# Performance work log

Hardware: AMD Instinct MI355X
Metric: run time of the kernel (lower is better)

## Reference

```python
import jax, jax.numpy as jnp
import numpy as np

N_HEAD = 16
N_EMBD = 1024
D_HEAD = N_EMBD // N_HEAD


def setup_inputs() -> dict:
    key = jax.random.key(0)
    ks = jax.random.split(key, 5)
    B, T, C = 4, 2048, N_EMBD
    s = 1.0 / np.sqrt(C)
    return {
        "x": jax.random.normal(ks[0], (B, T, C), dtype=jnp.float32),
        "w_qkv": jax.random.normal(ks[1], (C, 3 * C), dtype=jnp.float32) * s,
        "b_qkv": jnp.zeros((3 * C,), dtype=jnp.float32),
        "w_out": jax.random.normal(ks[2], (C, C), dtype=jnp.float32) * s,
        "b_out": jnp.zeros((C,), dtype=jnp.float32),
    }


def reference(x, w_qkv, b_qkv, w_out, b_out):
    B, T, C = x.shape
    qkv = x @ w_qkv + b_qkv  # [B,T,3C]
    q, k, v = jnp.split(qkv, 3, axis=-1)
    # [B,T,C] -> [B,H,T,D]
    def heads(t):
        return t.reshape(B, T, N_HEAD, D_HEAD).transpose(0, 2, 1, 3)
    q, k, v = heads(q), heads(k), heads(v)
    scores = jnp.einsum("bhqd,bhkd->bhqk", q, k) / np.sqrt(D_HEAD)
    causal = jnp.tril(jnp.ones((T, T), dtype=bool))
    scores = jnp.where(causal, scores, -jnp.inf)
    probs = jax.nn.softmax(scores, axis=-1)
    out = jnp.einsum("bhqk,bhkd->bhqd", probs, v)  # [B,H,T,D]
    out = out.transpose(0, 2, 1, 3).reshape(B, T, C)
    return out @ w_out + b_out
```

## Files before the change

kernel.cpp:

```cpp
#include <hip/hip_runtime.h>
#include <hip/hip_bf16.h>
#include <cstdint>
#include <cstddef>

typedef __attribute__((ext_vector_type(8))) short short8;
typedef __attribute__((ext_vector_type(4))) float f32x4;
typedef __attribute__((ext_vector_type(4))) uint16_t ushort4_t;
typedef __attribute__((ext_vector_type(4))) uint32_t uint4_t;

__device__ __forceinline__ uint16_t f2bf(float f) {
  union { float f; uint32_t u; } v; v.f = f;
  uint32_t r = v.u + 0x7FFFu + ((v.u >> 16) & 1u);
  return (uint16_t)(r >> 16);
}


__global__ __launch_bounds__(256) void cvt_f32_bf16(const float* __restrict__ in,
                                                    uint16_t* __restrict__ out, int n4) {
  int i = blockIdx.x * 256 + threadIdx.x;
  int stride = gridDim.x * 256;
  for (; i < n4; i += stride) {
    float4 v = ((const float4*)in)[i];
    ushort4_t o = { f2bf(v.x), f2bf(v.y), f2bf(v.z), f2bf(v.w) };
    ((ushort4_t*)out)[i] = o;
  }
}

__global__ __launch_bounds__(256) void transpose_cvt(const float* __restrict__ in,
                                                     uint16_t* __restrict__ out, int R, int C) {
  __shared__ float tile[32][33];
  int c0 = blockIdx.x * 32, r0 = blockIdx.y * 32;
  int tx = threadIdx.x, ty = threadIdx.y;
#pragma unroll
  for (int j = 0; j < 32; j += 8)
    tile[ty + j][tx] = in[(size_t)(r0 + ty + j) * C + c0 + tx];
  __syncthreads();
#pragma unroll
  for (int j = 0; j < 32; j += 8)
    out[(size_t)(c0 + ty + j) * R + r0 + tx] = f2bf(tile[tx][ty + j]);
}

__global__ __launch_bounds__(256) void transpose_v(const uint16_t* __restrict__ in,
                                                   uint16_t* __restrict__ out) {
  __shared__ uint16_t tile[32][33];
  int bh = blockIdx.z;
  int t0 = blockIdx.x * 32, d0 = blockIdx.y * 32;
  const uint16_t* ip = in + (size_t)bh * 2048 * 64;
  uint16_t* op = out + (size_t)bh * 64 * 2048;
  int tx = threadIdx.x, ty = threadIdx.y;
#pragma unroll
  for (int j = 0; j < 32; j += 8)
    tile[ty + j][tx] = ip[(size_t)(t0 + ty + j) * 64 + d0 + tx];
  __syncthreads();
  const int txp = (tx < 16) ? ((tx >> 2) * 8 + (tx & 3))
                            : (((tx - 16) >> 2) * 8 + 4 + (tx & 3));
#pragma unroll
  for (int j = 0; j < 32; j += 8)
    op[(size_t)(d0 + ty + j) * 2048 + t0 + txp] = tile[tx][ty + j];
}

__device__ __forceinline__ void stage16(const uint16_t* g, uint16_t* lds) {
  __builtin_amdgcn_global_load_lds((__attribute__((address_space(1))) void*)g,
                                   (__attribute__((address_space(3))) void*)lds, 16, 0, 0);
}

__global__ __launch_bounds__(256, 3) void gemm_qkv(
    const uint16_t* __restrict__ A, const uint16_t* __restrict__ Bt,
    const float* __restrict__ bias,
    uint16_t* __restrict__ q_out, uint16_t* __restrict__ k_out, uint16_t* __restrict__ v_out) {
  constexpr int K = 1024, KT = 16;
  __shared__ uint16_t lA[256 * 64];
  __shared__ uint16_t lB[128 * 64];
  const int tid = threadIdx.x;
  const int lane = tid & 63, w = tid >> 6;
  const int wm = w >> 1, wn = w & 1;
  const int r16 = lane & 15, hi = lane >> 4;
  const int wg = (blockIdx.x & 7) * 96 + (blockIdx.x >> 3);
  const int bm = wg / 24, bn = wg % 24;

  const int row0 = tid >> 3;
  const int cch0 = (tid & 7) ^ (row0 & 7);
  const uint16_t* aS = A + ((size_t)bm * 256 + row0) * K + cch0 * 8;
  const uint16_t* bS = Bt + ((size_t)bn * 128 + row0) * K + cch0 * 8;

  f32x4 acc[8][4];
#pragma unroll
  for (int m = 0; m < 8; ++m)
#pragma unroll
    for (int n = 0; n < 4; ++n) acc[m][n] = (f32x4){0.f, 0.f, 0.f, 0.f};

#pragma unroll 1
  for (int kt = 0; kt < KT; ++kt) {
#pragma unroll
    for (int it = 0; it < 8; ++it)
      stage16(aS + (size_t)(it * 32) * K + kt * 64, &lA[it * 2048 + tid * 8]);
#pragma unroll
    for (int it = 0; it < 4; ++it)
      stage16(bS + (size_t)(it * 32) * K + kt * 64, &lB[it * 2048 + tid * 8]);
    __syncthreads();

#pragma unroll
    for (int kk = 0; kk < 2; ++kk) {
      short8 bfr[4];
      const int swz = (kk * 64 + hi * 16) ^ ((r16 & 7) << 4);
#pragma unroll
      for (int n = 0; n < 4; ++n) {
        int rowb = wn * 64 + n * 16 + r16;
        bfr[n] = *(const short8*)((const char*)lB + rowb * 128 + swz);
      }
#pragma unroll
      for (int mh = 0; mh < 2; ++mh) {
        short8 af[4];
#pragma unroll
        for (int i = 0; i < 4; ++i) {
          int rowa = wm * 128 + mh * 64 + i * 16 + r16;
          af[i] = *(const short8*)((const char*)lA + rowa * 128 + swz);
        }
        __builtin_amdgcn_s_setprio(1);
#pragma unroll
        for (int i = 0; i < 4; ++i)
#pragma unroll
          for (int n = 0; n < 4; ++n)
            acc[mh * 4 + i][n] =
                __builtin_amdgcn_mfma_f32_16x16x32_bf16(af[i], bfr[n], acc[mh * 4 + i][n], 0, 0, 0);
        __builtin_amdgcn_s_setprio(0);
      }
    }
    __syncthreads();
  }

#pragma unroll
  for (int m = 0; m < 8; ++m) {
    int rg = bm * 256 + wm * 128 + (m >> 2) * 64 + (m & 3) * 16 + hi * 4;
#pragma unroll
    for (int n = 0; n < 4; ++n) {
      int cg = bn * 128 + wn * 64 + n * 16 + r16;
      float bv = bias[cg];
      int which = cg >> 10, hh = (cg >> 6) & 15, dd = cg & 63;
      uint16_t* dst = which == 0 ? q_out : (which == 1 ? k_out : v_out);
#pragma unroll
      for (int r = 0; r < 4; ++r) {
        int rgr = rg + r;
        dst[((size_t)((rgr >> 11) * 16 + hh) * 2048 + (rgr & 2047)) * 64 + dd] = f2bf(acc[m][n][r] + bv);
      }
    }
  }
}


__global__ __launch_bounds__(256) void gemm128_out(
    const uint16_t* __restrict__ A, const uint16_t* __restrict__ Bt,
    const float* __restrict__ bias, int K, float* __restrict__ f_out, int N) {
  __shared__ uint16_t lA[128 * 64];
  __shared__ uint16_t lB[128 * 64];
  const int tid = threadIdx.x;
  const int lane = tid & 63;
  const int w = tid >> 6, wm = w >> 1, wn = w & 1;
  const int r16 = lane & 15, hi = lane >> 4;
  const int bn = blockIdx.x, bm = blockIdx.y;

  f32x4 acc[4][4];
#pragma unroll
  for (int i = 0; i < 4; ++i)
#pragma unroll
    for (int j = 0; j < 4; ++j) acc[i][j] = (f32x4){0.f, 0.f, 0.f, 0.f};

  const int ksteps = K >> 6;
  for (int kt = 0; kt < ksteps; ++kt) {
#pragma unroll
    for (int it = 0; it < 4; ++it) {
      int ci = it * 256 + tid;
      int row = ci >> 3;
      int cch = (ci & 7) ^ (row & 7);
      stage16(A + (size_t)(bm * 128 + row) * K + kt * 64 + cch * 8, &lA[ci * 8]);
      stage16(Bt + (size_t)(bn * 128 + row) * K + kt * 64 + cch * 8, &lB[ci * 8]);
    }
    __syncthreads();
#pragma unroll
    for (int kk = 0; kk < 2; ++kk) {
      short8 af[4], bfr[4];
      int swz = (kk * 64 + hi * 16) ^ ((r16 & 7) << 4);
#pragma unroll
      for (int i = 0; i < 4; ++i) {
        int rowa = wm * 64 + i * 16 + r16;
        af[i] = *(const short8*)((const char*)lA + rowa * 128 + swz);
        int rowb = wn * 64 + i * 16 + r16;
        bfr[i] = *(const short8*)((const char*)lB + rowb * 128 + swz);
      }
#pragma unroll
      for (int i = 0; i < 4; ++i)
#pragma unroll
        for (int j = 0; j < 4; ++j)
          acc[i][j] = __builtin_amdgcn_mfma_f32_16x16x32_bf16(af[i], bfr[j], acc[i][j], 0, 0, 0);
    }
    __syncthreads();
  }

#pragma unroll
  for (int i = 0; i < 4; ++i) {
    int rbase = bm * 128 + wm * 64 + i * 16 + hi * 4;
#pragma unroll
    for (int j = 0; j < 4; ++j) {
      int cg = bn * 128 + wn * 64 + j * 16 + r16;
      float bv = bias[cg];
#pragma unroll
      for (int r = 0; r < 4; ++r)
        f_out[(size_t)(rbase + r) * N + cg] = acc[i][j][r] + bv;
    }
  }
}

__global__ __launch_bounds__(256, 3) void attn_fwd(
    const uint16_t* __restrict__ Qm, const uint16_t* __restrict__ Km,
    const uint16_t* __restrict__ Vt, uint16_t* __restrict__ O) {
  __shared__ uint16_t kbuf[2][64 * 64];
  __shared__ uint16_t vbuf[2][64 * 64];
  const int tid = threadIdx.x;
  const int lane = tid & 63, w = tid >> 6;
  const int r16 = lane & 15, hi = lane >> 4;
  const int bid = blockIdx.x;
  const int bh = (bid & 7) + 8 * ((bid >> 3) & 7);
  const int qb = 15 - (bid >> 6);
  const int b = bh >> 4, h = bh & 15;
  const size_t base = (size_t)bh * 2048 * 64;
  const int qlo = qb * 128 + w * 32;
  const int NT = 2 * qb + 2;

  const float SC = 0.18033688011112042f;
  const float BIAS = -20.197730572445487f;

  short8 ones8;
#pragma unroll
  for (int i = 0; i < 8; ++i) ones8[i] = (short)0x3F80;

  short8 aq[2][2];
#pragma unroll
  for (int st = 0; st < 2; ++st)
#pragma unroll
    for (int c = 0; c < 2; ++c)
      aq[st][c] = *(const short8*)&Qm[base + (size_t)(qlo + st * 16 + r16) * 64 + c * 32 + hi * 8];

  f32x4 o[2][4];
  f32x4 o4[2];
#pragma unroll
  for (int st = 0; st < 2; ++st) {
#pragma unroll
    for (int j = 0; j < 4; ++j) o[st][j] = (f32x4){0.f, 0.f, 0.f, 0.f};
    o4[st] = (f32x4){0.f, 0.f, 0.f, 0.f};
  }

  auto stage_tile = [&](int pb, int kv0) {
    {
      int c = tid;            int row = c >> 3, cch = (c & 7) ^ (row & 7);
      stage16(Km + base + (size_t)(kv0 + row) * 64 + cch * 8, &kbuf[pb][c * 8]);
    }
    {
      int c = tid + 256;      int row = c >> 3, cch = (c & 7) ^ (row & 7);
      stage16(Km + base + (size_t)(kv0 + row) * 64 + cch * 8, &kbuf[pb][c * 8]);
    }
    {
      int c = tid;            int row = c >> 3, cch = (c & 7) ^ (row & 7);
      stage16(Vt + base + (size_t)row * 2048 + kv0 + cch * 8, &vbuf[pb][c * 8]);
    }
    {
      int c = tid + 256;      int row = c >> 3, cch = (c & 7) ^ (row & 7);
      stage16(Vt + base + (size_t)row * 2048 + kv0 + cch * 8, &vbuf[pb][c * 8]);
    }
  };

  int pb = 0;
  stage_tile(0, 0);
#pragma unroll 1
  for (int t = 0; t < NT; ++t) {
    const int kv0 = t << 6;
    if (t + 1 < NT) {
      stage_tile(pb ^ 1, (t + 1) << 6);
      asm volatile("s_waitcnt vmcnt(4)" ::: "memory");
    } else {
      asm volatile("s_waitcnt vmcnt(0)" ::: "memory");
    }
    __builtin_amdgcn_s_barrier();
    __builtin_amdgcn_sched_barrier(0);

    if (kv0 <= qlo + 31) {
      const bool maskt = (kv0 + 64 > qlo);
      short8 bk[4][2];
#pragma unroll
      for (int ct = 0; ct < 4; ++ct)
#pragma unroll
        for (int c = 0; c < 2; ++c) {
          int row = ct * 16 + r16;
          int ch = (c * 4 + hi) ^ (row & 7);
          bk[ct][c] = *(const short8*)((const char*)&kbuf[pb][0] + row * 128 + ch * 16);
        }
      short8 bv[4][2];
#pragma unroll
      for (int j = 0; j < 4; ++j)
#pragma unroll
        for (int ks = 0; ks < 2; ++ks) {
          int row = j * 16 + r16;
          int ch = (ks * 4 + hi) ^ (row & 7);
          bv[j][ks] = *(const short8*)((const char*)&vbuf[pb][0] + row * 128 + ch * 16);
        }

#pragma unroll
      for (int st = 0; st < 2; ++st) {
        f32x4 sc[4];
#pragma unroll
        for (int ct = 0; ct < 4; ++ct) sc[ct] = (f32x4){0.f, 0.f, 0.f, 0.f};
        __builtin_amdgcn_s_setprio(1);
#pragma unroll
        for (int ct = 0; ct < 4; ++ct)
#pragma unroll
          for (int c = 0; c < 2; ++c)
            sc[ct] = __builtin_amdgcn_mfma_f32_16x16x32_bf16(bk[ct][c], aq[st][c], sc[ct], 0, 0, 0);
        __builtin_amdgcn_s_setprio(0);

        float p[4][4];
        const int qg = qlo + st * 16 + r16;
#pragma unroll
        for (int ct = 0; ct < 4; ++ct) {
          const int kb_ = kv0 + ct * 16 + hi * 4;
#pragma unroll
          for (int r = 0; r < 4; ++r) {
            float x = exp2f(fmaf(sc[ct][r], SC, BIAS));
            if (maskt && (kb_ + r > qg)) x = 0.f;
            p[ct][r] = x;
          }
        }

        short8 pf[2];
#pragma unroll
        for (int ks = 0; ks < 2; ++ks) {
          uint32_t d0, d1, d2, d3;
          asm("v_cvt_pk_bf16_f32 %0, %1, %2" : "=v"(d0) : "v"(p[2 * ks][0]), "v"(p[2 * ks][1]));
          asm("v_cvt_pk_bf16_f32 %0, %1, %2" : "=v"(d1) : "v"(p[2 * ks][2]), "v"(p[2 * ks][3]));
          asm("v_cvt_pk_bf16_f32 %0, %1, %2" : "=v"(d2) : "v"(p[2 * ks + 1][0]), "v"(p[2 * ks + 1][1]));
          asm("v_cvt_pk_bf16_f32 %0, %1, %2" : "=v"(d3) : "v"(p[2 * ks + 1][2]), "v"(p[2 * ks + 1][3]));
          uint4_t uu = { d0, d1, d2, d3 };
          pf[ks] = __builtin_bit_cast(short8, uu);
        }

        __builtin_amdgcn_s_setprio(1);
#pragma unroll
        for (int ks = 0; ks < 2; ++ks)
          o4[st] = __builtin_amdgcn_mfma_f32_16x16x32_bf16(ones8, pf[ks], o4[st], 0, 0, 0);
#pragma unroll
        for (int j = 0; j < 4; ++j)
#pragma unroll
          for (int ks = 0; ks < 2; ++ks)
            o[st][j] = __builtin_amdgcn_mfma_f32_16x16x32_bf16(bv[j][ks], pf[ks], o[st][j], 0, 0, 0);
        __builtin_amdgcn_s_setprio(0);
      }
    }

    __builtin_amdgcn_s_barrier();
    __builtin_amdgcn_sched_barrier(0);
    pb ^= 1;
  }

#pragma unroll
  for (int st = 0; st < 2; ++st) {
    float inv = 1.f / o4[st][0];
    int qg = qlo + st * 16 + r16;
    size_t rowo = ((size_t)(b * 2048 + qg)) * 1024 + h * 64;
#pragma unroll
    for (int j = 0; j < 4; ++j) {
      ushort4_t v4 = { f2bf(o[st][j][0] * inv), f2bf(o[st][j][1] * inv),
                       f2bf(o[st][j][2] * inv), f2bf(o[st][j][3] * inv) };
      *(ushort4_t*)&O[rowo + j * 16 + hi * 4] = v4;
    }
  }
}


extern "C" void kernel_launch(void* const* d_in, const int* in_sizes, int n_in,
                              void* d_out, int out_size, void* d_ws, size_t ws_size,
                              hipStream_t stream) {
  const float* x = (const float*)d_in[0];
  const float* w_qkv = (const float*)d_in[1];
  const float* b_qkv = (const float*)d_in[2];
  const float* w_out = (const float*)d_in[3];
  const float* b_out = (const float*)d_in[4];
  float* out = (float*)d_out;

  const size_t BT = 8192, C = 1024, N3 = 3072, BHTD = 8388608;
  char* p = (char*)d_ws;
  uint16_t* xbf = (uint16_t*)p;   p += BT * C * 2;
  uint16_t* wqkvT = (uint16_t*)p; p += N3 * C * 2;
  uint16_t* woutT = (uint16_t*)p; p += C * C * 2;
  uint16_t* qb = (uint16_t*)p;    p += BHTD * 2;
  uint16_t* kb = (uint16_t*)p;    p += BHTD * 2;
  uint16_t* vb = (uint16_t*)p;    p += BHTD * 2;
  uint16_t* vtb = (uint16_t*)p;   p += BHTD * 2;
  uint16_t* ob = (uint16_t*)p;    p += BHTD * 2;

  cvt_f32_bf16<<<2048, 256, 0, stream>>>(x, xbf, (int)(BT * C / 4));
  transpose_cvt<<<dim3(96, 32), dim3(32, 8), 0, stream>>>(w_qkv, wqkvT, 1024, 3072);
  transpose_cvt<<<dim3(32, 32), dim3(32, 8), 0, stream>>>(w_out, woutT, 1024, 1024);
  gemm_qkv<<<768, 256, 0, stream>>>(xbf, wqkvT, b_qkv, qb, kb, vb);
  transpose_v<<<dim3(64, 2, 64), dim3(32, 8), 0, stream>>>(vb, vtb);
  attn_fwd<<<1024, 256, 0, stream>>>(qb, kb, vtb, ob);
  gemm128_out<<<dim3(8, 64), 256, 0, stream>>>(ob, woutT, b_out, 1024, out, 1024);
}
```

Measured before the change: 198.1 us.

## Fuse V transpose into QKV GEMM epilogue and use intrinsic bf16 conversion

The QKV GEMM epilogue now writes V straight into the transposed, permuted layout the attention kernel expects, using 4-element vector stores. This removes the separate transpose_v kernel and its extra round trip of V through global memory. Separately, the attention kernel's inline-asm packed bf16 conversion is replaced by per-element __float2bfloat16 calls, which may or may not lower to the same packed instruction. The strided scattered V stores in the epilogue could be less coalesced than before.

```diff
diff --git a/kernel.cpp b/kernel.cpp
--- a/kernel.cpp
+++ b/kernel.cpp
@@ -6,12 +6,17 @@
 typedef __attribute__((ext_vector_type(8))) short short8;
 typedef __attribute__((ext_vector_type(4))) float f32x4;
 typedef __attribute__((ext_vector_type(4))) uint16_t ushort4_t;
-typedef __attribute__((ext_vector_type(4))) uint32_t uint4_t;
 
 __device__ __forceinline__ uint16_t f2bf(float f) {
   union { float f; uint32_t u; } v; v.f = f;
   uint32_t r = v.u + 0x7FFFu + ((v.u >> 16) & 1u);
   return (uint16_t)(r >> 16);
+}
+
+__device__ __forceinline__ uint16_t f2bf_hw(float f) {
+  union { __hip_bfloat16 h; uint16_t u; } cv;
+  cv.h = __float2bfloat16(f);
+  return cv.u;
 }
 
 
@@ -40,25 +45,6 @@
     out[(size_t)(c0 + ty + j) * R + r0 + tx] = f2bf(tile[tx][ty + j]);
 }
 
-__global__ __launch_bounds__(256) void transpose_v(const uint16_t* __restrict__ in,
-                                                   uint16_t* __restrict__ out) {
-  __shared__ uint16_t tile[32][33];
-  int bh = blockIdx.z;
-  int t0 = blockIdx.x * 32, d0 = blockIdx.y * 32;
-  const uint16_t* ip = in + (size_t)bh * 2048 * 64;
-  uint16_t* op = out + (size_t)bh * 64 * 2048;
-  int tx = threadIdx.x, ty = threadIdx.y;
-#pragma unroll
-  for (int j = 0; j < 32; j += 8)
-    tile[ty + j][tx] = ip[(size_t)(t0 + ty + j) * 64 + d0 + tx];
-  __syncthreads();
-  const int txp = (tx < 16) ? ((tx >> 2) * 8 + (tx & 3))
-                            : (((tx - 16) >> 2) * 8 + 4 + (tx & 3));
-#pragma unroll
-  for (int j = 0; j < 32; j += 8)
-    op[(size_t)(d0 + ty + j) * 2048 + t0 + txp] = tile[tx][ty + j];
-}
-
 __device__ __forceinline__ void stage16(const uint16_t* g, uint16_t* lds) {
   __builtin_amdgcn_global_load_lds((__attribute__((address_space(1))) void*)g,
                                    (__attribute__((address_space(3))) void*)lds, 16, 0, 0);
@@ -67,7 +53,7 @@
 __global__ __launch_bounds__(256, 3) void gemm_qkv(
     const uint16_t* __restrict__ A, const uint16_t* __restrict__ Bt,
     const float* __restrict__ bias,
-    uint16_t* __restrict__ q_out, uint16_t* __restrict__ k_out, uint16_t* __restrict__ v_out) {
+    uint16_t* __restrict__ q_out, uint16_t* __restrict__ k_out, uint16_t* __restrict__ vt_out) {
   constexpr int K = 1024, KT = 16;
   __shared__ uint16_t lA[256 * 64];
   __shared__ uint16_t lB[128 * 64];
@@ -137,11 +123,19 @@
       int cg = bn * 128 + wn * 64 + n * 16 + r16;
       float bv = bias[cg];
       int which = cg >> 10, hh = (cg >> 6) & 15, dd = cg & 63;
-      uint16_t* dst = which == 0 ? q_out : (which == 1 ? k_out : v_out);
-#pragma unroll
-      for (int r = 0; r < 4; ++r) {
-        int rgr = rg + r;
-        dst[((size_t)((rgr >> 11) * 16 + hh) * 2048 + (rgr & 2047)) * 64 + dd] = f2bf(acc[m][n][r] + bv);
+      if (which == 2) {
+        int bb = rg >> 11, tt = rg & 2047, tx = tt & 31;
+        int txp = (tx < 16) ? ((tx >> 2) * 8) : (((tx - 16) >> 2) * 8 + 4);
+        ushort4_t v4 = { f2bf(acc[m][n][0] + bv), f2bf(acc[m][n][1] + bv),
+                         f2bf(acc[m][n][2] + bv), f2bf(acc[m][n][3] + bv) };
+        *(ushort4_t*)&vt_out[((size_t)(bb * 16 + hh) * 64 + dd) * 2048 + (tt & ~31) + txp] = v4;
+      } else {
+        uint16_t* dst = which == 0 ? q_out : k_out;
+#pragma unroll
+        for (int r = 0; r < 4; ++r) {
+          int rgr = rg + r;
+          dst[((size_t)((rgr >> 11) * 16 + hh) * 2048 + (rgr & 2047)) * 64 + dd] = f2bf(acc[m][n][r] + bv);
+        }
       }
     }
   }
@@ -332,13 +326,12 @@
         short8 pf[2];
 #pragma unroll
         for (int ks = 0; ks < 2; ++ks) {
-          uint32_t d0, d1, d2, d3;
-          asm("v_cvt_pk_bf16_f32 %0, %1, %2" : "=v"(d0) : "v"(p[2 * ks][0]), "v"(p[2 * ks][1]));
-          asm("v_cvt_pk_bf16_f32 %0, %1, %2" : "=v"(d1) : "v"(p[2 * ks][2]), "v"(p[2 * ks][3]));
-          asm("v_cvt_pk_bf16_f32 %0, %1, %2" : "=v"(d2) : "v"(p[2 * ks + 1][0]), "v"(p[2 * ks + 1][1]));
-          asm("v_cvt_pk_bf16_f32 %0, %1, %2" : "=v"(d3) : "v"(p[2 * ks + 1][2]), "v"(p[2 * ks + 1][3]));
-          uint4_t uu = { d0, d1, d2, d3 };
-          pf[ks] = __builtin_bit_cast(short8, uu);
+          short8 t8;
+#pragma unroll
+          for (int r = 0; r < 4; ++r) t8[r] = (short)f2bf_hw(p[2 * ks][r]);
+#pragma unroll
+          for (int r = 0; r < 4; ++r) t8[4 + r] = (short)f2bf_hw(p[2 * ks + 1][r]);
+          pf[ks] = t8;
         }
 
         __builtin_amdgcn_s_setprio(1);
@@ -391,15 +384,13 @@
   uint16_t* woutT = (uint16_t*)p; p += C * C * 2;
   uint16_t* qb = (uint16_t*)p;    p += BHTD * 2;
   uint16_t* kb = (uint16_t*)p;    p += BHTD * 2;
-  uint16_t* vb = (uint16_t*)p;    p += BHTD * 2;
   uint16_t* vtb = (uint16_t*)p;   p += BHTD * 2;
   uint16_t* ob = (uint16_t*)p;    p += BHTD * 2;
 
   cvt_f32_bf16<<<2048, 256, 0, stream>>>(x, xbf, (int)(BT * C / 4));
   transpose_cvt<<<dim3(96, 32), dim3(32, 8), 0, stream>>>(w_qkv, wqkvT, 1024, 3072);
   transpose_cvt<<<dim3(32, 32), dim3(32, 8), 0, stream>>>(w_out, woutT, 1024, 1024);
-  gemm_qkv<<<768, 256, 0, stream>>>(xbf, wqkvT, b_qkv, qb, kb, vb);
-  transpose_v<<<dim3(64, 2, 64), dim3(32, 8), 0, stream>>>(vb, vtb);
+  gemm_qkv<<<768, 256, 0, stream>>>(xbf, wqkvT, b_qkv, qb, kb, vtb);
   attn_fwd<<<1024, 256, 0, stream>>>(qb, kb, vtb, ob);
   gemm128_out<<<dim3(8, 64), 256, 0, stream>>>(ob, woutT, b_out, 1024, out, 1024);
 }
```

Result: faster. 192.6 us (-2.8%).
